# Performance work log

Hardware: AMD Instinct MI355X
Metric: run time of the kernel (lower is better)

The kernel has to match this reference:

```python
import jax, jax.numpy as jnp
import numpy as np

N = 65536          # nodes
E = 1048576        # edges
IN_C = 128
HID_C = 32
HEADS = 4
OUT_C = 64
NEG_SLOPE = 0.2
EPS = 1e-16


def gat_conv(x, edge_index, W, att_src, att_dst, bias, heads, out_c, concat):
    """PyG-style GATConv. x: [N, F_in]; edge_index: [2, E] (row=src, col=dst).
    W: [F_in, heads*out_c]; att_src/att_dst: [heads, out_c]; bias: [heads*out_c] or [out_c]."""
    src, dst = edge_index[0], edge_index[1]
    n = x.shape[0]
    h = (x @ W).reshape(n, heads, out_c)                      # [N, H, C]
    a_src = jnp.einsum('nhc,hc->nh', h, att_src)              # [N, H]
    a_dst = jnp.einsum('nhc,hc->nh', h, att_dst)              # [N, H]
    alpha = a_src[src] + a_dst[dst]                           # [E, H]
    alpha = jax.nn.leaky_relu(alpha, NEG_SLOPE)
    # segment softmax over incoming edges of each destination node
    amax = jax.ops.segment_max(alpha, dst, num_segments=n)    # [N, H]
    alpha = jnp.exp(alpha - amax[dst])
    denom = jax.ops.segment_sum(alpha, dst, num_segments=n)   # [N, H]
    alpha = alpha / (denom[dst] + EPS)
    # weighted scatter-add aggregation
    msgs = alpha[:, :, None] * h[src]                         # [E, H, C]
    out = jax.ops.segment_sum(msgs, dst, num_segments=n)      # [N, H, C]
    if concat:
        out = out.reshape(n, heads * out_c)
    else:
        out = out.mean(axis=1)
    return out + bias


def setup_inputs() -> dict:
    key = jax.random.key(0)
    ks = jax.random.split(key, 10)
    s_in = 1.0 / np.sqrt(IN_C)
    s_h = 1.0 / np.sqrt(HEADS * HID_C)
    x = jax.random.normal(ks[0], (N, IN_C), dtype=jnp.float32)
    edge_index = jax.random.randint(ks[1], (2, E), 0, N, dtype=jnp.int64)
    W1 = jax.random.normal(ks[2], (IN_C, HEADS * HID_C), dtype=jnp.float32) * s_in
    att_src1 = jax.random.normal(ks[3], (HEADS, HID_C), dtype=jnp.float32) * s_h
    att_dst1 = jax.random.normal(ks[4], (HEADS, HID_C), dtype=jnp.float32) * s_h
    b1 = jnp.zeros((HEADS * HID_C,), dtype=jnp.float32)
    W2 = jax.random.normal(ks[5], (HEADS * HID_C, OUT_C), dtype=jnp.float32) * s_h
    att_src2 = jax.random.normal(ks[6], (1, OUT_C), dtype=jnp.float32) * s_h
    att_dst2 = jax.random.normal(ks[7], (1, OUT_C), dtype=jnp.float32) * s_h
    b2 = jnp.zeros((OUT_C,), dtype=jnp.float32)
    return {"x": x, "edge_index": edge_index, "W1": W1, "att_src1": att_src1,
            "att_dst1": att_dst1, "b1": b1, "W2": W2, "att_src2": att_src2,
            "att_dst2": att_dst2, "b2": b2}


def reference(x, edge_index, W1, att_src1, att_dst1, b1, W2, att_src2, att_dst2, b2):
    # dropout is identity in eval mode
    h = gat_conv(x, edge_index, W1, att_src1, att_dst1, b1, HEADS, HID_C, concat=True)
    h = jax.nn.sigmoid(h)
    h = gat_conv(h, edge_index, W2, att_src2, att_dst2, b2, 1, OUT_C, concat=True)
    return jax.nn.sigmoid(h)
```

## Files before the change

### kernel.cpp

```cpp
#include <hip/hip_runtime.h>
#include <hip/hip_fp16.h>

#define N_NODES 65536
#define N_EDGES 1048576
#define NBUCK 256
#define PBLOCKS 256
#define EPB (N_EDGES / PBLOCKS)
#define K4CAP 6144
constexpr float NEG = 0.2f;
constexpr float EPS_ = 1e-16f;
constexpr float WSHIFT = 2.7725887f;

typedef __attribute__((ext_vector_type(8))) short bf16x8;
typedef __attribute__((ext_vector_type(4))) float f32x4;

__device__ __forceinline__ unsigned short f2bf(float f) {
    unsigned int u = __float_as_uint(f);
    return (unsigned short)((u + 0x7fffu + ((u >> 16) & 1u)) >> 16);
}
__device__ __forceinline__ unsigned short f2h(float f) {
    __half_raw r = __half_raw(__float2half(f));
    return r.x;
}
__device__ __forceinline__ __half2 u2h2(unsigned int u) {
    union { unsigned int u; __half2 h; } c; c.u = u; return c.h;
}
__device__ __forceinline__ unsigned int h22u(__half2 h) {
    union { unsigned int u; __half2 h; } c; c.h = h; return c.u;
}
__device__ __forceinline__ float lrelu_exp_s(float l) {
    return __expf(fmaxf(l, NEG * l) - WSHIFT);
}


__global__ __launch_bounds__(256) void coarse_hist(const int* __restrict__ ei,
                                                   int* __restrict__ hist_mat) {
    __shared__ int h[NBUCK];
    int t = threadIdx.x;
    h[t] = 0;
    __syncthreads();
    int base = blockIdx.x * EPB;
    #pragma unroll
    for (int i = 0; i < EPB / 256; ++i) {
        int d = ei[N_EDGES + base + i * 256 + t];
        atomicAdd(&h[d >> 8], 1);
    }
    __syncthreads();
    hist_mat[t * PBLOCKS + blockIdx.x] = h[t];
}

__global__ __launch_bounds__(1024) void scan_a(const int* __restrict__ in,
                                               int* __restrict__ out,
                                               int* __restrict__ bsum) {
    __shared__ int sm[1024];
    int t = threadIdx.x, i = blockIdx.x * 1024 + t;
    int v = in[i];
    sm[t] = v;
    __syncthreads();
    for (int off = 1; off < 1024; off <<= 1) {
        int u = (t >= off) ? sm[t - off] : 0;
        __syncthreads();
        sm[t] += u;
        __syncthreads();
    }
    out[i] = sm[t] - v;
    if (t == 1023) bsum[blockIdx.x] = sm[t];
}

__global__ __launch_bounds__(1024) void scan_c(int* __restrict__ arr,
                                               const int* __restrict__ bsum) {
    __shared__ int off[64];
    int t = threadIdx.x;
    if (t < 64) {
        int v = bsum[t];
        int incl = v;
        #pragma unroll
        for (int o = 1; o < 64; o <<= 1) {
            int u = __shfl_up(incl, o);
            if (t >= o) incl += u;
        }
        off[t] = incl - v;
    }
    __syncthreads();
    int i = blockIdx.x * 1024 + t;
    arr[i] += off[blockIdx.x];
}

__global__ __launch_bounds__(256) void partition_kernel(const int* __restrict__ ei,
                                                        const int* __restrict__ cursor_mat,
                                                        unsigned int* __restrict__ edge_part) {
    __shared__ int h[NBUCK];
    __shared__ int start[NBUCK];
    __shared__ int cur[NBUCK];
    __shared__ int gcur[NBUCK];
    __shared__ unsigned int stage[EPB];
    int t = threadIdx.x;
    h[t] = 0;
    gcur[t] = cursor_mat[t * PBLOCKS + blockIdx.x];
    __syncthreads();
    unsigned int ent[EPB / 256];
    int base = blockIdx.x * EPB;
    #pragma unroll
    for (int i = 0; i < EPB / 256; ++i) {
        int e = base + i * 256 + t;
        int s = ei[e], d = ei[N_EDGES + e];
        ent[i] = ((unsigned int)s << 16) | (unsigned int)d;
        atomicAdd(&h[d >> 8], 1);
    }
    __syncthreads();
    int v = h[t];
    start[t] = v;
    __syncthreads();
    for (int off = 1; off < 256; off <<= 1) {
        int u = (t >= off) ? start[t - off] : 0;
        __syncthreads();
        start[t] += u;
        __syncthreads();
    }
    int excl = start[t] - v;
    start[t] = excl;
    cur[t] = excl;
    __syncthreads();
    #pragma unroll
    for (int i = 0; i < EPB / 256; ++i) {
        int b = (int)((ent[i] & 0xffffu) >> 8);
        int slot = atomicAdd(&cur[b], 1);
        stage[slot] = ent[i];
    }
    __syncthreads();
    int s0 = t * (EPB / 256);
    #pragma unroll
    for (int i = 0; i < EPB / 256; ++i) {
        unsigned int p = stage[s0 + i];
        int b = (int)((p & 0xffffu) >> 8);
        edge_part[gcur[b] + (s0 + i - start[b])] = p;
    }
}

__global__ __launch_bounds__(256) void finalize_kernel(const unsigned int* __restrict__ edge_part,
                                                       const int* __restrict__ cursor_mat,
                                                       int* __restrict__ row_ptr,
                                                       int* __restrict__ csr_src) {
    __shared__ int h[256];
    __shared__ int sc[256];
    __shared__ int cur[256];
    __shared__ unsigned short stage[K4CAP];
    int t = threadIdx.x;
    int b = blockIdx.x;
    if (b == NBUCK - 1 && t == 0) row_ptr[N_NODES] = N_EDGES;
    int cs = cursor_mat[b * PBLOCKS];
    int ce = (b == NBUCK - 1) ? N_EDGES : cursor_mat[(b + 1) * PBLOCKS];
    int cnt = ce - cs;
    h[t] = 0;
    __syncthreads();
    for (int i = t; i < cnt; i += 256)
        atomicAdd(&h[edge_part[cs + i] & 0xffu], 1);
    __syncthreads();
    int v = h[t];
    sc[t] = v;
    __syncthreads();
    for (int off = 1; off < 256; off <<= 1) {
        int u = (t >= off) ? sc[t - off] : 0;
        __syncthreads();
        sc[t] += u;
        __syncthreads();
    }
    int excl = sc[t] - v;
    row_ptr[b * 256 + t] = cs + excl;
    cur[t] = excl;
    __syncthreads();
    if (cnt <= K4CAP) {
        for (int i = t; i < cnt; i += 256) {
            unsigned int p = edge_part[cs + i];
            int slot = atomicAdd(&cur[p & 0xffu], 1);
            stage[slot] = (unsigned short)(p >> 16);
        }
        __syncthreads();
        for (int i = t; i < cnt; i += 256)
            csr_src[cs + i] = (int)stage[i];
    } else {
        for (int i = t; i < cnt; i += 256) {
            unsigned int p = edge_part[cs + i];
            int slot = atomicAdd(&cur[p & 0xffu], 1);
            csr_src[cs + slot] = (int)(p >> 16);
        }
    }
}


__global__ __launch_bounds__(256) void gemm1_mfma(const float* __restrict__ X,
                                                  const float* __restrict__ W,
                                                  unsigned short* __restrict__ H) {
    constexpr int OUTC = 128;
    constexpr int NT = OUTC / 16;
    extern __shared__ unsigned short Wl[];
    int t = threadIdx.x;
    for (int idx = t; idx < OUTC * 128; idx += 256) {
        int j = idx & 7;
        int ln = (idx >> 3) & 63;
        int fc = idx >> 9;
        int kc = fc & 3, ct = fc >> 2;
        int k = kc * 32 + (ln >> 4) * 8 + j;
        int n = ct * 16 + (ln & 15);
        Wl[idx] = (unsigned short)f2bf(W[k * OUTC + n]);
    }
    __syncthreads();
    int wave = t >> 6, lane = t & 63;
    int m = lane & 15, quad = lane >> 4;
    int node_base = blockIdx.x * 64 + wave * 16;
    const float* xrow = X + (size_t)(node_base + m) * 128 + quad * 8;
    bf16x8 a[4];
    #pragma unroll
    for (int kc = 0; kc < 4; ++kc) {
        float4 u = *(const float4*)(xrow + kc * 32);
        float4 v = *(const float4*)(xrow + kc * 32 + 4);
        bf16x8 af;
        af[0] = (short)f2bf(u.x); af[1] = (short)f2bf(u.y);
        af[2] = (short)f2bf(u.z); af[3] = (short)f2bf(u.w);
        af[4] = (short)f2bf(v.x); af[5] = (short)f2bf(v.y);
        af[6] = (short)f2bf(v.z); af[7] = (short)f2bf(v.w);
        a[kc] = af;
    }
    #pragma unroll
    for (int ct = 0; ct < NT; ++ct) {
        f32x4 acc = {0.f, 0.f, 0.f, 0.f};
        #pragma unroll
        for (int kc = 0; kc < 4; ++kc) {
            bf16x8 bfr = *(const bf16x8*)(Wl + ((ct * 4 + kc) * 64 + lane) * 8);
            acc = __builtin_amdgcn_mfma_f32_16x16x32_bf16(a[kc], bfr, acc, 0, 0, 0);
        }
        #pragma unroll
        for (int r = 0; r < 4; ++r) {
            int row = quad * 4 + r;
            H[(size_t)(node_base + row) * OUTC + ct * 16 + m] = f2h(acc[r]);
        }
    }
}


__global__ __launch_bounds__(256) void gemm2_mfma(const unsigned short* __restrict__ X,
                                                  const float* __restrict__ W,
                                                  unsigned short* __restrict__ H) {
    constexpr int OUTC = 64;
    constexpr int NT = OUTC / 16;
    extern __shared__ unsigned short Wl[];
    int t = threadIdx.x;
    for (int idx = t; idx < OUTC * 128; idx += 256) {
        int j = idx & 7;
        int ln = (idx >> 3) & 63;
        int fc = idx >> 9;
        int kc = fc & 3, ct = fc >> 2;
        int k = kc * 32 + (ln >> 4) * 8 + j;
        int n = ct * 16 + (ln & 15);
        Wl[idx] = (unsigned short)f2bf(W[k * OUTC + n]);
    }
    __syncthreads();
    int wave = t >> 6, lane = t & 63;
    int m = lane & 15, quad = lane >> 4;
    int node_base = blockIdx.x * 64 + wave * 16;
    const unsigned short* xrow = X + (size_t)(node_base + m) * 128 + quad * 8;
    bf16x8 a[4];
    #pragma unroll
    for (int kc = 0; kc < 4; ++kc) a[kc] = *(const bf16x8*)(xrow + kc * 32);
    #pragma unroll
    for (int ct = 0; ct < NT; ++ct) {
        f32x4 acc = {0.f, 0.f, 0.f, 0.f};
        #pragma unroll
        for (int kc = 0; kc < 4; ++kc) {
            bf16x8 bfr = *(const bf16x8*)(Wl + ((ct * 4 + kc) * 64 + lane) * 8);
            acc = __builtin_amdgcn_mfma_f32_16x16x32_bf16(a[kc], bfr, acc, 0, 0, 0);
        }
        #pragma unroll
        for (int r = 0; r < 4; ++r) {
            int row = quad * 4 + r;
            H[(size_t)(node_base + row) * OUTC + ct * 16 + m] = f2h(acc[r]);
        }
    }
}


__global__ __launch_bounds__(256) void att1_kernel(const unsigned int* __restrict__ h1u,
                                                   const float* __restrict__ as_w,
                                                   const float* __restrict__ ad_w,
                                                   float* __restrict__ a_src,
                                                   float* __restrict__ a_dst) {
    int wave = (blockIdx.x * 256 + threadIdx.x) >> 6;
    int lane = threadIdx.x & 63;
    __half2 p = u2h2(h1u[wave * 64 + lane]);
    float h0 = __low2float(p), h1v = __high2float(p);
    float2 sw = *(const float2*)(as_w + lane * 2);
    float2 dw = *(const float2*)(ad_w + lane * 2);
    float ps = h0 * sw.x + h1v * sw.y;
    float pd = h0 * dw.x + h1v * dw.y;
    #pragma unroll
    for (int m = 1; m < 16; m <<= 1) {
        ps += __shfl_xor(ps, m);
        pd += __shfl_xor(pd, m);
    }
    if ((lane & 15) == 0) {
        a_src[wave * 4 + (lane >> 4)] = ps;
        a_dst[wave * 4 + (lane >> 4)] = pd;
    }
}

__global__ __launch_bounds__(256) void att2_kernel(const __half* __restrict__ h2h,
                                                   const float* __restrict__ as_w,
                                                   const float* __restrict__ ad_w,
                                                   float* __restrict__ a_src,
                                                   float* __restrict__ a_dst) {
    int wave = (blockIdx.x * 256 + threadIdx.x) >> 6;
    int lane = threadIdx.x & 63;
    float v = __half2float(h2h[wave * 64 + lane]);
    float ps = v * as_w[lane];
    float pd = v * ad_w[lane];
    #pragma unroll
    for (int m = 1; m < 64; m <<= 1) {
        ps += __shfl_xor(ps, m);
        pd += __shfl_xor(pd, m);
    }
    if (lane == 0) {
        a_src[wave] = ps;
        a_dst[wave] = pd;
    }
}


__global__ __launch_bounds__(256) void agg1_kernel(const int* __restrict__ row_ptr,
                                                   const int* __restrict__ csr_src,
                                                   const unsigned int* __restrict__ h1u,
                                                   const float* __restrict__ a_src,
                                                   const float* __restrict__ a_dst,
                                                   const float* __restrict__ b1,
                                                   unsigned short* __restrict__ x2) {
    int wave = (blockIdx.x * 256 + threadIdx.x) >> 6;
    int lane = threadIdx.x & 63;
    int half = lane >> 5;
    int ln = lane & 31;
    int n = wave * 2 + half;
    int j8 = ln & 7;
    int whead = ln >> 3;
    int sub = ln >> 4;
    int col = ln & 15;
    int hd_c = col >> 2;
    int rbase = half * 32 + hd_c * 8 + sub;
    float adw = a_dst[n * 4 + whead];
    int e = row_ptr[n], end = row_ptr[n + 1];
    __half2 acc0 = u2h2(0u), acc1 = u2h2(0u), acc2 = u2h2(0u), acc3 = u2h2(0u);
    float denom = 0.f;
    while (e < end) {
        int mb = end - e;
        if (mb > 8) mb = 8;
        int s_l = csr_src[e + (j8 < mb ? j8 : 0)];
        float l = a_src[s_l * 4 + whead] + adw;
        float wv = (j8 < mb) ? lrelu_exp_s(l) : 0.f;
        denom += wv;
        unsigned int pack = ((unsigned int)f2h(wv) << 16) | (unsigned int)s_l;
        #pragma unroll
        for (int g = 0; g < 4; ++g) {
            unsigned int pk = __shfl(pack, rbase + g * 2);
            unsigned int wu = pk >> 16;
            __half2 w2 = u2h2(wu | (wu << 16));
            unsigned int s = pk & 0xffffu;
            uint4 hv = *(const uint4*)(h1u + s * 64 + col * 4);
            acc0 = __hfma2(w2, u2h2(hv.x), acc0);
            acc1 = __hfma2(w2, u2h2(hv.y), acc1);
            acc2 = __hfma2(w2, u2h2(hv.z), acc2);
            acc3 = __hfma2(w2, u2h2(hv.w), acc3);
        }
        e += 8;
    }
    acc0 = __hadd2(acc0, u2h2(__shfl_xor(h22u(acc0), 16)));
    acc1 = __hadd2(acc1, u2h2(__shfl_xor(h22u(acc1), 16)));
    acc2 = __hadd2(acc2, u2h2(__shfl_xor(h22u(acc2), 16)));
    acc3 = __hadd2(acc3, u2h2(__shfl_xor(h22u(acc3), 16)));
    #pragma unroll
    for (int m = 1; m < 8; m <<= 1) denom += __shfl_xor(denom, m);
    float dfin = __shfl(denom, half * 32 + hd_c * 8);
    if (sub == 0) {
        float inv = 1.f / (dfin + EPS_);
        int c0 = col * 8;
        float v[8];
        v[0] = __low2float(acc0); v[1] = __high2float(acc0);
        v[2] = __low2float(acc1); v[3] = __high2float(acc1);
        v[4] = __low2float(acc2); v[5] = __high2float(acc2);
        v[6] = __low2float(acc3); v[7] = __high2float(acc3);
        unsigned int o[4];
        #pragma unroll
        for (int i = 0; i < 4; ++i) {
            float u0 = v[2 * i] * inv + b1[c0 + 2 * i];
            float u1 = v[2 * i + 1] * inv + b1[c0 + 2 * i + 1];
            u0 = 1.f / (1.f + __expf(-u0));
            u1 = 1.f / (1.f + __expf(-u1));
            o[i] = (unsigned int)f2bf(u0) | ((unsigned int)f2bf(u1) << 16);
        }
        *(uint4*)(x2 + (size_t)n * 128 + c0) = make_uint4(o[0], o[1], o[2], o[3]);
    }
}


__global__ __launch_bounds__(256) void agg2_kernel(const int* __restrict__ row_ptr,
                                                   const int* __restrict__ csr_src,
                                                   const unsigned int* __restrict__ h2u,
                                                   const float* __restrict__ a_src,
                                                   const float* __restrict__ a_dst,
                                                   const float* __restrict__ b2,
                                                   float* __restrict__ out) {
    int wave = (blockIdx.x * 256 + threadIdx.x) >> 6;
    int lane = threadIdx.x & 63;
    int half = lane >> 5;
    int ln = lane & 31;
    int n = wave * 2 + half;
    int j8 = ln & 7;
    int sub = (ln >> 3) & 3;
    int col = ln & 7;
    int rbase = half * 32 + sub;
    float ad = a_dst[n];
    int e = row_ptr[n], end = row_ptr[n + 1];
    __half2 acc0 = u2h2(0u), acc1 = u2h2(0u), acc2 = u2h2(0u), acc3 = u2h2(0u);
    float denom = 0.f;
    while (e < end) {
        int mb = end - e;
        if (mb > 8) mb = 8;
        int s_l = csr_src[e + (j8 < mb ? j8 : 0)];
        float l = a_src[s_l] + ad;
        float wv = (j8 < mb) ? lrelu_exp_s(l) : 0.f;
        denom += wv;
        unsigned int pack = ((unsigned int)f2h(wv) << 16) | (unsigned int)s_l;
        #pragma unroll
        for (int g = 0; g < 2; ++g) {
            unsigned int pk = __shfl(pack, rbase + g * 4);
            unsigned int wu = pk >> 16;
            __half2 w2 = u2h2(wu | (wu << 16));
            unsigned int s = pk & 0xffffu;
            uint4 hv = *(const uint4*)(h2u + s * 32 + col * 4);
            acc0 = __hfma2(w2, u2h2(hv.x), acc0);
            acc1 = __hfma2(w2, u2h2(hv.y), acc1);
            acc2 = __hfma2(w2, u2h2(hv.z), acc2);
            acc3 = __hfma2(w2, u2h2(hv.w), acc3);
        }
        e += 8;
    }
    #pragma unroll
    for (int m = 8; m < 32; m <<= 1) {
        acc0 = __hadd2(acc0, u2h2(__shfl_xor(h22u(acc0), m)));
        acc1 = __hadd2(acc1, u2h2(__shfl_xor(h22u(acc1), m)));
        acc2 = __hadd2(acc2, u2h2(__shfl_xor(h22u(acc2), m)));
        acc3 = __hadd2(acc3, u2h2(__shfl_xor(h22u(acc3), m)));
    }
    #pragma unroll
    for (int m = 1; m < 8; m <<= 1) denom += __shfl_xor(denom, m);
    if (sub == 0) {
        float inv = 1.f / (denom + EPS_);
        int c0 = col * 8;
        float v[8];
        v[0] = __low2float(acc0); v[1] = __high2float(acc0);
        v[2] = __low2float(acc1); v[3] = __high2float(acc1);
        v[4] = __low2float(acc2); v[5] = __high2float(acc2);
        v[6] = __low2float(acc3); v[7] = __high2float(acc3);
        float o[8];
        #pragma unroll
        for (int i = 0; i < 8; ++i) {
            float u = v[i] * inv + b2[c0 + i];
            o[i] = 1.f / (1.f + __expf(-u));
        }
        float4* dst = (float4*)(out + (size_t)n * 64 + c0);
        dst[0] = make_float4(o[0], o[1], o[2], o[3]);
        dst[1] = make_float4(o[4], o[5], o[6], o[7]);
    }
}


extern "C" void kernel_launch(void* const* d_in, const int* in_sizes, int n_in,
                              void* d_out, int out_size, void* d_ws, size_t ws_size,
                              hipStream_t stream) {
    (void)in_sizes; (void)n_in; (void)out_size; (void)ws_size;
    const float* x   = (const float*)d_in[0];
    const int*   ei  = (const int*)d_in[1];
    const float* W1  = (const float*)d_in[2];
    const float* as1 = (const float*)d_in[3];
    const float* ad1 = (const float*)d_in[4];
    const float* b1  = (const float*)d_in[5];
    const float* W2  = (const float*)d_in[6];
    const float* as2 = (const float*)d_in[7];
    const float* ad2 = (const float*)d_in[8];
    const float* b2  = (const float*)d_in[9];
    float* out = (float*)d_out;

    char* p = (char*)d_ws;
    auto alloc = [&](size_t bytes) -> void* {
        void* r = (void*)p;
        p += (bytes + 255) & ~(size_t)255;
        return r;
    };
    int* hist_mat   = (int*)alloc((size_t)NBUCK * PBLOCKS * 4);
    int* cursor_mat = (int*)alloc((size_t)NBUCK * PBLOCKS * 4);
    int* bsum       = (int*)alloc(64 * 4);
    unsigned int* edge_part = (unsigned int*)alloc((size_t)N_EDGES * 4);
    int* row_ptr    = (int*)alloc((size_t)(N_NODES + 1) * 4);
    int* csr_src    = (int*)alloc((size_t)N_EDGES * 4);
    unsigned short* h1 = (unsigned short*)alloc((size_t)N_NODES * 128 * 2);
    float* a_src1   = (float*)alloc((size_t)N_NODES * 4 * 4);
    float* a_dst1   = (float*)alloc((size_t)N_NODES * 4 * 4);
    unsigned short* x2 = (unsigned short*)alloc((size_t)N_NODES * 128 * 2);
    unsigned short* h2 = (unsigned short*)alloc((size_t)N_NODES * 64 * 2);
    float* a_src2   = (float*)alloc((size_t)N_NODES * 4);
    float* a_dst2   = (float*)alloc((size_t)N_NODES * 4);

    coarse_hist<<<PBLOCKS, 256, 0, stream>>>(ei, hist_mat);
    scan_a<<<64, 1024, 0, stream>>>(hist_mat, cursor_mat, bsum);
    scan_c<<<64, 1024, 0, stream>>>(cursor_mat, bsum);
    partition_kernel<<<PBLOCKS, 256, 0, stream>>>(ei, cursor_mat, edge_part);
    finalize_kernel<<<NBUCK, 256, 0, stream>>>(edge_part, cursor_mat, row_ptr, csr_src);

    gemm1_mfma<<<N_NODES / 64, 256, 128 * 128 * 2, stream>>>(x, W1, h1);
    att1_kernel<<<N_NODES / 4, 256, 0, stream>>>((const unsigned int*)h1, as1, ad1, a_src1, a_dst1);
    agg1_kernel<<<N_NODES / 8, 256, 0, stream>>>(row_ptr, csr_src, (const unsigned int*)h1,
                                                 a_src1, a_dst1, b1, x2);

    gemm2_mfma<<<N_NODES / 64, 256, 128 * 64 * 2, stream>>>(x2, W2, h2);
    att2_kernel<<<N_NODES / 4, 256, 0, stream>>>((const __half*)h2, as2, ad2, a_src2, a_dst2);
    agg2_kernel<<<N_NODES / 8, 256, 0, stream>>>(row_ptr, csr_src, (const unsigned int*)h2,
                                                 a_src2, a_dst2, b2, out);
}
```

Before: 249.0 us.

## Store node features head-major and split aggregation blocks per head/channel slice

Feature tables h1, x2 and h2 are now stored as separate per-head (or per-32-channel) planes instead of interleaved per node. The aggregation kernels launch one block per (node group, head/slice), so each gathered row is a 64-byte slice from a smaller table. This is meant to improve cache locality of the random gathers, since each plane is a quarter or half the size of the full table. The cost is re-reading the CSR and attention scores once per head or slice, and launching more blocks.

```diff
diff --git a/kernel.cpp b/kernel.cpp
--- a/kernel.cpp
+++ b/kernel.cpp
@@ -229,10 +229,12 @@
             bf16x8 bfr = *(const bf16x8*)(Wl + ((ct * 4 + kc) * 64 + lane) * 8);
             acc = __builtin_amdgcn_mfma_f32_16x16x32_bf16(a[kc], bfr, acc, 0, 0, 0);
         }
+        int ch = ct * 16 + m;
+        int hd = ch >> 5, c32 = ch & 31;
         #pragma unroll
         for (int r = 0; r < 4; ++r) {
             int row = quad * 4 + r;
-            H[(size_t)(node_base + row) * OUTC + ct * 16 + m] = f2h(acc[r]);
+            H[((size_t)hd * N_NODES + node_base + row) * 32 + c32] = f2h(acc[r]);
         }
     }
 }
@@ -258,10 +260,10 @@
     int wave = t >> 6, lane = t & 63;
     int m = lane & 15, quad = lane >> 4;
     int node_base = blockIdx.x * 64 + wave * 16;
-    const unsigned short* xrow = X + (size_t)(node_base + m) * 128 + quad * 8;
     bf16x8 a[4];
     #pragma unroll
-    for (int kc = 0; kc < 4; ++kc) a[kc] = *(const bf16x8*)(xrow + kc * 32);
+    for (int kc = 0; kc < 4; ++kc)
+        a[kc] = *(const bf16x8*)(X + ((size_t)kc * N_NODES + node_base + m) * 32 + quad * 8);
     #pragma unroll
     for (int ct = 0; ct < NT; ++ct) {
         f32x4 acc = {0.f, 0.f, 0.f, 0.f};
@@ -270,10 +272,12 @@
             bf16x8 bfr = *(const bf16x8*)(Wl + ((ct * 4 + kc) * 64 + lane) * 8);
             acc = __builtin_amdgcn_mfma_f32_16x16x32_bf16(a[kc], bfr, acc, 0, 0, 0);
         }
+        int ch = ct * 16 + m;
+        int cs = ch >> 5, c32 = ch & 31;
         #pragma unroll
         for (int r = 0; r < 4; ++r) {
             int row = quad * 4 + r;
-            H[(size_t)(node_base + row) * OUTC + ct * 16 + m] = f2h(acc[r]);
+            H[((size_t)cs * N_NODES + node_base + row) * 32 + c32] = f2h(acc[r]);
         }
     }
 }
@@ -284,9 +288,9 @@
                                                    const float* __restrict__ ad_w,
                                                    float* __restrict__ a_src,
                                                    float* __restrict__ a_dst) {
-    int wave = (blockIdx.x * 256 + threadIdx.x) >> 6;
+    int node = (blockIdx.x * 256 + threadIdx.x) >> 6;
     int lane = threadIdx.x & 63;
-    __half2 p = u2h2(h1u[wave * 64 + lane]);
+    __half2 p = u2h2(h1u[((size_t)(lane >> 4) * N_NODES + node) * 16 + (lane & 15)]);
     float h0 = __low2float(p), h1v = __high2float(p);
     float2 sw = *(const float2*)(as_w + lane * 2);
     float2 dw = *(const float2*)(ad_w + lane * 2);
@@ -298,8 +302,8 @@
         pd += __shfl_xor(pd, m);
     }
     if ((lane & 15) == 0) {
-        a_src[wave * 4 + (lane >> 4)] = ps;
-        a_dst[wave * 4 + (lane >> 4)] = pd;
+        a_src[node * 4 + (lane >> 4)] = ps;
+        a_dst[node * 4 + (lane >> 4)] = pd;
     }
 }
 
@@ -308,9 +312,9 @@
                                                    const float* __restrict__ ad_w,
                                                    float* __restrict__ a_src,
                                                    float* __restrict__ a_dst) {
-    int wave = (blockIdx.x * 256 + threadIdx.x) >> 6;
+    int node = (blockIdx.x * 256 + threadIdx.x) >> 6;
     int lane = threadIdx.x & 63;
-    float v = __half2float(h2h[wave * 64 + lane]);
+    float v = __half2float(h2h[((size_t)(lane >> 5) * N_NODES + node) * 32 + (lane & 31)]);
     float ps = v * as_w[lane];
     float pd = v * ad_w[lane];
     #pragma unroll
@@ -319,31 +323,31 @@
         pd += __shfl_xor(pd, m);
     }
     if (lane == 0) {
-        a_src[wave] = ps;
-        a_dst[wave] = pd;
+        a_src[node] = ps;
+        a_dst[node] = pd;
     }
 }
 
 
 __global__ __launch_bounds__(256) void agg1_kernel(const int* __restrict__ row_ptr,
                                                    const int* __restrict__ csr_src,
-                                                   const unsigned int* __restrict__ h1u,
+                                                   const unsigned short* __restrict__ h1hm,
                                                    const float* __restrict__ a_src,
                                                    const float* __restrict__ a_dst,
                                                    const float* __restrict__ b1,
-                                                   unsigned short* __restrict__ x2) {
-    int wave = (blockIdx.x * 256 + threadIdx.x) >> 6;
-    int lane = threadIdx.x & 63;
+                                                   unsigned short* __restrict__ x2hm) {
+    int head = blockIdx.x & 3;
+    int nb = blockIdx.x >> 2;
+    int t = threadIdx.x;
+    int lane = t & 63;
     int half = lane >> 5;
     int ln = lane & 31;
-    int n = wave * 2 + half;
+    int n = nb * 8 + (t >> 6) * 2 + half;
     int j8 = ln & 7;
-    int whead = ln >> 3;
-    int sub = ln >> 4;
-    int col = ln & 15;
-    int hd_c = col >> 2;
-    int rbase = half * 32 + hd_c * 8 + sub;
-    float adw = a_dst[n * 4 + whead];
+    int slot = ln >> 2;
+    int li = ln & 3;
+    const unsigned short* tbl = h1hm + (size_t)head * N_NODES * 32;
+    float adw = a_dst[n * 4 + head];
     int e = row_ptr[n], end = row_ptr[n + 1];
     __half2 acc0 = u2h2(0u), acc1 = u2h2(0u), acc2 = u2h2(0u), acc3 = u2h2(0u);
     float denom = 0.f;
@@ -351,34 +355,33 @@
         int mb = end - e;
         if (mb > 8) mb = 8;
         int s_l = csr_src[e + (j8 < mb ? j8 : 0)];
-        float l = a_src[s_l * 4 + whead] + adw;
+        float l = a_src[s_l * 4 + head] + adw;
         float wv = (j8 < mb) ? lrelu_exp_s(l) : 0.f;
         denom += wv;
         unsigned int pack = ((unsigned int)f2h(wv) << 16) | (unsigned int)s_l;
-        #pragma unroll
-        for (int g = 0; g < 4; ++g) {
-            unsigned int pk = __shfl(pack, rbase + g * 2);
-            unsigned int wu = pk >> 16;
-            __half2 w2 = u2h2(wu | (wu << 16));
-            unsigned int s = pk & 0xffffu;
-            uint4 hv = *(const uint4*)(h1u + s * 64 + col * 4);
-            acc0 = __hfma2(w2, u2h2(hv.x), acc0);
-            acc1 = __hfma2(w2, u2h2(hv.y), acc1);
-            acc2 = __hfma2(w2, u2h2(hv.z), acc2);
-            acc3 = __hfma2(w2, u2h2(hv.w), acc3);
-        }
+        unsigned int pk = __shfl(pack, half * 32 + slot);
+        unsigned int wu = pk >> 16;
+        __half2 w2 = u2h2(wu | (wu << 16));
+        unsigned int s = pk & 0xffffu;
+        uint4 hv = *(const uint4*)(tbl + (size_t)s * 32 + li * 8);
+        acc0 = __hfma2(w2, u2h2(hv.x), acc0);
+        acc1 = __hfma2(w2, u2h2(hv.y), acc1);
+        acc2 = __hfma2(w2, u2h2(hv.z), acc2);
+        acc3 = __hfma2(w2, u2h2(hv.w), acc3);
         e += 8;
     }
-    acc0 = __hadd2(acc0, u2h2(__shfl_xor(h22u(acc0), 16)));
-    acc1 = __hadd2(acc1, u2h2(__shfl_xor(h22u(acc1), 16)));
-    acc2 = __hadd2(acc2, u2h2(__shfl_xor(h22u(acc2), 16)));
-    acc3 = __hadd2(acc3, u2h2(__shfl_xor(h22u(acc3), 16)));
+    #pragma unroll
+    for (int m = 4; m < 32; m <<= 1) {
+        acc0 = __hadd2(acc0, u2h2(__shfl_xor(h22u(acc0), m)));
+        acc1 = __hadd2(acc1, u2h2(__shfl_xor(h22u(acc1), m)));
+        acc2 = __hadd2(acc2, u2h2(__shfl_xor(h22u(acc2), m)));
+        acc3 = __hadd2(acc3, u2h2(__shfl_xor(h22u(acc3), m)));
+    }
     #pragma unroll
     for (int m = 1; m < 8; m <<= 1) denom += __shfl_xor(denom, m);
-    float dfin = __shfl(denom, half * 32 + hd_c * 8);
-    if (sub == 0) {
-        float inv = 1.f / (dfin + EPS_);
-        int c0 = col * 8;
+    if (slot == 0) {
+        float inv = 1.f / (denom + EPS_);
+        int c0 = li * 8;
         float v[8];
         v[0] = __low2float(acc0); v[1] = __high2float(acc0);
         v[2] = __low2float(acc1); v[3] = __high2float(acc1);
@@ -387,33 +390,36 @@
         unsigned int o[4];
         #pragma unroll
         for (int i = 0; i < 4; ++i) {
-            float u0 = v[2 * i] * inv + b1[c0 + 2 * i];
-            float u1 = v[2 * i + 1] * inv + b1[c0 + 2 * i + 1];
+            float u0 = v[2 * i] * inv + b1[head * 32 + c0 + 2 * i];
+            float u1 = v[2 * i + 1] * inv + b1[head * 32 + c0 + 2 * i + 1];
             u0 = 1.f / (1.f + __expf(-u0));
             u1 = 1.f / (1.f + __expf(-u1));
             o[i] = (unsigned int)f2bf(u0) | ((unsigned int)f2bf(u1) << 16);
         }
-        *(uint4*)(x2 + (size_t)n * 128 + c0) = make_uint4(o[0], o[1], o[2], o[3]);
+        *(uint4*)(x2hm + ((size_t)head * N_NODES + n) * 32 + c0) =
+            make_uint4(o[0], o[1], o[2], o[3]);
     }
 }
 
 
 __global__ __launch_bounds__(256) void agg2_kernel(const int* __restrict__ row_ptr,
                                                    const int* __restrict__ csr_src,
-                                                   const unsigned int* __restrict__ h2u,
+                                                   const unsigned short* __restrict__ h2cs,
                                                    const float* __restrict__ a_src,
                                                    const float* __restrict__ a_dst,
                                                    const float* __restrict__ b2,
                                                    float* __restrict__ out) {
-    int wave = (blockIdx.x * 256 + threadIdx.x) >> 6;
-    int lane = threadIdx.x & 63;
+    int cs = blockIdx.x & 1;
+    int nb = blockIdx.x >> 1;
+    int t = threadIdx.x;
+    int lane = t & 63;
     int half = lane >> 5;
     int ln = lane & 31;
-    int n = wave * 2 + half;
+    int n = nb * 8 + (t >> 6) * 2 + half;
     int j8 = ln & 7;
-    int sub = (ln >> 3) & 3;
-    int col = ln & 7;
-    int rbase = half * 32 + sub;
+    int slot = ln >> 2;
+    int li = ln & 3;
+    const unsigned short* tbl = h2cs + (size_t)cs * N_NODES * 32;
     float ad = a_dst[n];
     int e = row_ptr[n], end = row_ptr[n + 1];
     __half2 acc0 = u2h2(0u), acc1 = u2h2(0u), acc2 = u2h2(0u), acc3 = u2h2(0u);
@@ -426,22 +432,19 @@
         float wv = (j8 < mb) ? lrelu_exp_s(l) : 0.f;
         denom += wv;
         unsigned int pack = ((unsigned int)f2h(wv) << 16) | (unsigned int)s_l;
-        #pragma unroll
-        for (int g = 0; g < 2; ++g) {
-            unsigned int pk = __shfl(pack, rbase + g * 4);
-            unsigned int wu = pk >> 16;
-            __half2 w2 = u2h2(wu | (wu << 16));
-            unsigned int s = pk & 0xffffu;
-            uint4 hv = *(const uint4*)(h2u + s * 32 + col * 4);
-            acc0 = __hfma2(w2, u2h2(hv.x), acc0);
-            acc1 = __hfma2(w2, u2h2(hv.y), acc1);
-            acc2 = __hfma2(w2, u2h2(hv.z), acc2);
-            acc3 = __hfma2(w2, u2h2(hv.w), acc3);
-        }
+        unsigned int pk = __shfl(pack, half * 32 + slot);
+        unsigned int wu = pk >> 16;
+        __half2 w2 = u2h2(wu | (wu << 16));
+        unsigned int s = pk & 0xffffu;
+        uint4 hv = *(const uint4*)(tbl + (size_t)s * 32 + li * 8);
+        acc0 = __hfma2(w2, u2h2(hv.x), acc0);
+        acc1 = __hfma2(w2, u2h2(hv.y), acc1);
+        acc2 = __hfma2(w2, u2h2(hv.z), acc2);
+        acc3 = __hfma2(w2, u2h2(hv.w), acc3);
         e += 8;
     }
     #pragma unroll
-    for (int m = 8; m < 32; m <<= 1) {
+    for (int m = 4; m < 32; m <<= 1) {
         acc0 = __hadd2(acc0, u2h2(__shfl_xor(h22u(acc0), m)));
         acc1 = __hadd2(acc1, u2h2(__shfl_xor(h22u(acc1), m)));
         acc2 = __hadd2(acc2, u2h2(__shfl_xor(h22u(acc2), m)));
@@ -449,9 +452,9 @@
     }
     #pragma unroll
     for (int m = 1; m < 8; m <<= 1) denom += __shfl_xor(denom, m);
-    if (sub == 0) {
+    if (slot == 0) {
         float inv = 1.f / (denom + EPS_);
-        int c0 = col * 8;
+        int c0 = cs * 32 + li * 8;
         float v[8];
         v[0] = __low2float(acc0); v[1] = __high2float(acc0);
         v[2] = __low2float(acc1); v[3] = __high2float(acc1);
@@ -514,11 +517,11 @@
 
     gemm1_mfma<<<N_NODES / 64, 256, 128 * 128 * 2, stream>>>(x, W1, h1);
     att1_kernel<<<N_NODES / 4, 256, 0, stream>>>((const unsigned int*)h1, as1, ad1, a_src1, a_dst1);
-    agg1_kernel<<<N_NODES / 8, 256, 0, stream>>>(row_ptr, csr_src, (const unsigned int*)h1,
-                                                 a_src1, a_dst1, b1, x2);
+    agg1_kernel<<<(N_NODES / 8) * 4, 256, 0, stream>>>(row_ptr, csr_src, h1,
+                                                       a_src1, a_dst1, b1, x2);
 
     gemm2_mfma<<<N_NODES / 64, 256, 128 * 64 * 2, stream>>>(x2, W2, h2);
     att2_kernel<<<N_NODES / 4, 256, 0, stream>>>((const __half*)h2, as2, ad2, a_src2, a_dst2);
-    agg2_kernel<<<N_NODES / 8, 256, 0, stream>>>(row_ptr, csr_src, (const unsigned int*)h2,
-                                                 a_src2, a_dst2, b2, out);
-}
+    agg2_kernel<<<(N_NODES / 8) * 2, 256, 0, stream>>>(row_ptr, csr_src, h2,
+                                                       a_src2, a_dst2, b2, out);
+}
```

Result: slower. 311.8 us (+25.2%).

## Widen CSR build parallelism and store source indices as 16-bit

Applied to the files above, without the earlier changes.

Raises the partition block count from 256 to 1024, which makes the histogram matrix larger. A three-level scan (scan_a, a new single-block scan_b, scan_c) replaces the old two-level one to cover it. Finalize now runs 1024 threads per bucket, and CSR source indices are stored as uint16, since node ids fit in 16 bits, which halves the index traffic read by both aggregation kernels. The cost is an extra scan launch and four times as many cursor entries; partition blocks now handle only 1024 edges each, so each block does less work.

```diff
diff --git a/kernel.cpp b/kernel.cpp
--- a/kernel.cpp
+++ b/kernel.cpp
@@ -4,7 +4,7 @@
 #define N_NODES 65536
 #define N_EDGES 1048576
 #define NBUCK 256
-#define PBLOCKS 256
+#define PBLOCKS 1024
 #define EPB (N_EDGES / PBLOCKS)
 #define K4CAP 6144
 constexpr float NEG = 0.2f;
@@ -67,23 +67,25 @@
     if (t == 1023) bsum[blockIdx.x] = sm[t];
 }
 
+__global__ __launch_bounds__(256) void scan_b(int* __restrict__ bsum) {
+    __shared__ int sm[256];
+    int t = threadIdx.x;
+    int v = bsum[t];
+    sm[t] = v;
+    __syncthreads();
+    for (int off = 1; off < 256; off <<= 1) {
+        int u = (t >= off) ? sm[t - off] : 0;
+        __syncthreads();
+        sm[t] += u;
+        __syncthreads();
+    }
+    bsum[t] = sm[t] - v;
+}
+
 __global__ __launch_bounds__(1024) void scan_c(int* __restrict__ arr,
                                                const int* __restrict__ bsum) {
-    __shared__ int off[64];
-    int t = threadIdx.x;
-    if (t < 64) {
-        int v = bsum[t];
-        int incl = v;
-        #pragma unroll
-        for (int o = 1; o < 64; o <<= 1) {
-            int u = __shfl_up(incl, o);
-            if (t >= o) incl += u;
-        }
-        off[t] = incl - v;
-    }
-    __syncthreads();
-    int i = blockIdx.x * 1024 + t;
-    arr[i] += off[blockIdx.x];
+    int i = blockIdx.x * 1024 + threadIdx.x;
+    arr[i] += bsum[blockIdx.x];
 }
 
 __global__ __launch_bounds__(256) void partition_kernel(const int* __restrict__ ei,
@@ -137,10 +139,10 @@
     }
 }
 
-__global__ __launch_bounds__(256) void finalize_kernel(const unsigned int* __restrict__ edge_part,
-                                                       const int* __restrict__ cursor_mat,
-                                                       int* __restrict__ row_ptr,
-                                                       int* __restrict__ csr_src) {
+__global__ __launch_bounds__(1024) void finalize_kernel(const unsigned int* __restrict__ edge_part,
+                                                        const int* __restrict__ cursor_mat,
+                                                        int* __restrict__ row_ptr,
+                                                        unsigned short* __restrict__ csr16) {
     __shared__ int h[256];
     __shared__ int sc[256];
     __shared__ int cur[256];
@@ -151,38 +153,40 @@
     int cs = cursor_mat[b * PBLOCKS];
     int ce = (b == NBUCK - 1) ? N_EDGES : cursor_mat[(b + 1) * PBLOCKS];
     int cnt = ce - cs;
-    h[t] = 0;
-    __syncthreads();
-    for (int i = t; i < cnt; i += 256)
+    if (t < 256) h[t] = 0;
+    __syncthreads();
+    for (int i = t; i < cnt; i += 1024)
         atomicAdd(&h[edge_part[cs + i] & 0xffu], 1);
     __syncthreads();
-    int v = h[t];
-    sc[t] = v;
+    int v = 0;
+    if (t < 256) { v = h[t]; sc[t] = v; }
     __syncthreads();
     for (int off = 1; off < 256; off <<= 1) {
-        int u = (t >= off) ? sc[t - off] : 0;
-        __syncthreads();
-        sc[t] += u;
-        __syncthreads();
-    }
-    int excl = sc[t] - v;
-    row_ptr[b * 256 + t] = cs + excl;
-    cur[t] = excl;
+        int u = (t < 256 && t >= off) ? sc[t - off] : 0;
+        __syncthreads();
+        if (t < 256) sc[t] += u;
+        __syncthreads();
+    }
+    if (t < 256) {
+        int excl = sc[t] - v;
+        row_ptr[b * 256 + t] = cs + excl;
+        cur[t] = excl;
+    }
     __syncthreads();
     if (cnt <= K4CAP) {
-        for (int i = t; i < cnt; i += 256) {
+        for (int i = t; i < cnt; i += 1024) {
             unsigned int p = edge_part[cs + i];
             int slot = atomicAdd(&cur[p & 0xffu], 1);
             stage[slot] = (unsigned short)(p >> 16);
         }
         __syncthreads();
-        for (int i = t; i < cnt; i += 256)
-            csr_src[cs + i] = (int)stage[i];
+        for (int i = t; i < cnt; i += 1024)
+            csr16[cs + i] = stage[i];
     } else {
-        for (int i = t; i < cnt; i += 256) {
+        for (int i = t; i < cnt; i += 1024) {
             unsigned int p = edge_part[cs + i];
             int slot = atomicAdd(&cur[p & 0xffu], 1);
-            csr_src[cs + slot] = (int)(p >> 16);
+            csr16[cs + slot] = (unsigned short)(p >> 16);
         }
     }
 }
@@ -326,7 +330,7 @@
 
 
 __global__ __launch_bounds__(256) void agg1_kernel(const int* __restrict__ row_ptr,
-                                                   const int* __restrict__ csr_src,
+                                                   const unsigned short* __restrict__ csr16,
                                                    const unsigned int* __restrict__ h1u,
                                                    const float* __restrict__ a_src,
                                                    const float* __restrict__ a_dst,
@@ -350,7 +354,7 @@
     while (e < end) {
         int mb = end - e;
         if (mb > 8) mb = 8;
-        int s_l = csr_src[e + (j8 < mb ? j8 : 0)];
+        int s_l = (int)csr16[e + (j8 < mb ? j8 : 0)];
         float l = a_src[s_l * 4 + whead] + adw;
         float wv = (j8 < mb) ? lrelu_exp_s(l) : 0.f;
         denom += wv;
@@ -397,9 +401,8 @@
     }
 }
 
-
 __global__ __launch_bounds__(256) void agg2_kernel(const int* __restrict__ row_ptr,
-                                                   const int* __restrict__ csr_src,
+                                                   const unsigned short* __restrict__ csr16,
                                                    const unsigned int* __restrict__ h2u,
                                                    const float* __restrict__ a_src,
                                                    const float* __restrict__ a_dst,
@@ -421,7 +424,7 @@
     while (e < end) {
         int mb = end - e;
         if (mb > 8) mb = 8;
-        int s_l = csr_src[e + (j8 < mb ? j8 : 0)];
+        int s_l = (int)csr16[e + (j8 < mb ? j8 : 0)];
         float l = a_src[s_l] + ad;
         float wv = (j8 < mb) ? lrelu_exp_s(l) : 0.f;
         denom += wv;
@@ -494,10 +497,10 @@
     };
     int* hist_mat   = (int*)alloc((size_t)NBUCK * PBLOCKS * 4);
     int* cursor_mat = (int*)alloc((size_t)NBUCK * PBLOCKS * 4);
-    int* bsum       = (int*)alloc(64 * 4);
+    int* bsum       = (int*)alloc(256 * 4);
     unsigned int* edge_part = (unsigned int*)alloc((size_t)N_EDGES * 4);
     int* row_ptr    = (int*)alloc((size_t)(N_NODES + 1) * 4);
-    int* csr_src    = (int*)alloc((size_t)N_EDGES * 4);
+    unsigned short* csr16 = (unsigned short*)alloc((size_t)N_EDGES * 2);
     unsigned short* h1 = (unsigned short*)alloc((size_t)N_NODES * 128 * 2);
     float* a_src1   = (float*)alloc((size_t)N_NODES * 4 * 4);
     float* a_dst1   = (float*)alloc((size_t)N_NODES * 4 * 4);
@@ -507,18 +510,19 @@
     float* a_dst2   = (float*)alloc((size_t)N_NODES * 4);
 
     coarse_hist<<<PBLOCKS, 256, 0, stream>>>(ei, hist_mat);
-    scan_a<<<64, 1024, 0, stream>>>(hist_mat, cursor_mat, bsum);
-    scan_c<<<64, 1024, 0, stream>>>(cursor_mat, bsum);
+    scan_a<<<NBUCK * PBLOCKS / 1024, 1024, 0, stream>>>(hist_mat, cursor_mat, bsum);
+    scan_b<<<1, 256, 0, stream>>>(bsum);
+    scan_c<<<NBUCK * PBLOCKS / 1024, 1024, 0, stream>>>(cursor_mat, bsum);
     partition_kernel<<<PBLOCKS, 256, 0, stream>>>(ei, cursor_mat, edge_part);
-    finalize_kernel<<<NBUCK, 256, 0, stream>>>(edge_part, cursor_mat, row_ptr, csr_src);
+    finalize_kernel<<<NBUCK, 1024, 0, stream>>>(edge_part, cursor_mat, row_ptr, csr16);
 
     gemm1_mfma<<<N_NODES / 64, 256, 128 * 128 * 2, stream>>>(x, W1, h1);
     att1_kernel<<<N_NODES / 4, 256, 0, stream>>>((const unsigned int*)h1, as1, ad1, a_src1, a_dst1);
-    agg1_kernel<<<N_NODES / 8, 256, 0, stream>>>(row_ptr, csr_src, (const unsigned int*)h1,
+    agg1_kernel<<<N_NODES / 8, 256, 0, stream>>>(row_ptr, csr16, (const unsigned int*)h1,
                                                  a_src1, a_dst1, b1, x2);
 
     gemm2_mfma<<<N_NODES / 64, 256, 128 * 64 * 2, stream>>>(x2, W2, h2);
     att2_kernel<<<N_NODES / 4, 256, 0, stream>>>((const __half*)h2, as2, ad2, a_src2, a_dst2);
-    agg2_kernel<<<N_NODES / 8, 256, 0, stream>>>(row_ptr, csr_src, (const unsigned int*)h2,
+    agg2_kernel<<<N_NODES / 8, 256, 0, stream>>>(row_ptr, csr16, (const unsigned int*)h2,
                                                  a_src2, a_dst2, b2, out);
 }
```

Measured after the change: 244.8 us. Within noise of the previous version (-1.7%).
